# Kernel tuning notes

Hardware: AMD Instinct MI355X
Metric: run time of the kernel (lower is better)

## Reference

```python
import jax, jax.numpy as jnp
import numpy as np

N = 40000      # nodes
E = 640000     # edges
G = 64         # graphs in batch
F_IN = 128
H = 128


def setup_inputs() -> dict:
    key = jax.random.key(0)
    ks = jax.random.split(key, 10)
    x = jax.random.normal(ks[0], (N, F_IN), dtype=jnp.float32)
    edge_index = jax.random.randint(ks[1], (2, E), 0, N, dtype=jnp.int64)
    batch = jnp.sort(jax.random.randint(ks[2], (N,), 0, G, dtype=jnp.int64))
    s = 0.05
    W1 = jax.random.normal(ks[3], (F_IN, H), dtype=jnp.float32) * s
    W2 = jax.random.normal(ks[4], (H, H), dtype=jnp.float32) * s
    W3 = jax.random.normal(ks[5], (H, H), dtype=jnp.float32) * s
    Wl = jax.random.normal(ks[6], (H, 1), dtype=jnp.float32) * s
    b1 = jnp.zeros((H,), jnp.float32)
    b2 = jnp.zeros((H,), jnp.float32)
    b3 = jnp.zeros((H,), jnp.float32)
    bl = jnp.zeros((1,), jnp.float32)
    return {"x": x, "edge_index": edge_index, "batch": batch, "dropout_rate": 0,
            "W1": W1, "b1": b1, "W2": W2, "b2": b2, "W3": W3, "b3": b3,
            "Wl": Wl, "bl": bl}


def _gcn_norm(edge_index, n):
    # PyG GCNConv default: add self-loops, symmetric deg^{-1/2} normalization.
    loop = jnp.arange(n, dtype=edge_index.dtype)
    row = jnp.concatenate([edge_index[0], loop])  # source
    col = jnp.concatenate([edge_index[1], loop])  # target
    ones = jnp.ones(row.shape[0], jnp.float32)
    deg = jax.ops.segment_sum(ones, col, num_segments=n)
    dis = jnp.where(deg > 0, jax.lax.rsqrt(deg), 0.0)
    norm = dis[row] * dis[col]  # [E+N]
    return row, col, norm


def _gcn_conv(x, row, col, norm, W, b, n):
    h = x @ W + b                       # dense transform [N,H]
    msg = h[row] * norm[:, None]        # gather + scale  [E+N,H]
    return jax.ops.segment_sum(msg, col, num_segments=n)


def reference(x, edge_index, batch, dropout_rate, W1, b1, W2, b2, W3, b3, Wl, bl):
    n = x.shape[0]
    row, col, norm = _gcn_norm(edge_index, n)
    # eval mode: dropout(p=dropout_rate, training=False) is identity
    h = jax.nn.relu(_gcn_conv(x, row, col, norm, W1, b1, n))
    h = jax.nn.relu(_gcn_conv(h, row, col, norm, W2, b2, n))
    h = jax.nn.relu(_gcn_conv(h, row, col, norm, W3, b3, n))
    # global mean pool over graphs
    sums = jax.ops.segment_sum(h, batch, num_segments=G)           # [G,H]
    cnt = jax.ops.segment_sum(jnp.ones(n, jnp.float32), batch, num_segments=G)
    pooled = sums / jnp.maximum(cnt, 1.0)[:, None]
    return pooled @ Wl + bl             # [G,1]
```

## Files before the change

kernel.cpp:

```cpp
#include <hip/hip_runtime.h>

constexpr int N = 40000;
constexpr int E = 640000;
constexpr int G = 64;
constexpr int H = 128;

constexpr int NB      = (N + 255) / 256;
constexpr int EB      = (E + 255) / 256;
constexpr int GEMM1_B = N / 64;
constexpr int FUSED_B = N / 32;
constexpr int POOL_B  = N / 32;
constexpr int CSR_MAX = E + 8 * N;
constexpr int ZQ = CSR_MAX / 4 - 2;

typedef float    floatx2 __attribute__((ext_vector_type(2)));
typedef float    f32x4   __attribute__((ext_vector_type(4)));
typedef _Float16 f16x8   __attribute__((ext_vector_type(8)));

__device__ __forceinline__ unsigned pack_fp8x4(float a, float b, float c, float d) {
    unsigned v = 0;
    v = __builtin_amdgcn_cvt_pk_fp8_f32(a, b, v, false);
    v = __builtin_amdgcn_cvt_pk_fp8_f32(c, d, v, true);
    return v;
}

__device__ __forceinline__ void pk_fma(floatx2& acc, floatx2 a, floatx2 w2) {
    asm("v_pk_fma_f32 %0, %1, %2, %0" : "+v"(acc) : "v"(a), "v"(w2));
}

__device__ __forceinline__ void fma8p(floatx2& aclo, floatx2& achi, unsigned r, float w) {
    floatx2 lo = __builtin_amdgcn_cvt_pk_f32_fp8(r, false);
    floatx2 hi = __builtin_amdgcn_cvt_pk_f32_fp8(r, true);
    floatx2 w2 = {w, w};
    pk_fma(aclo, lo, w2);
    pk_fma(achi, hi, w2);
}

__device__ __forceinline__ float entry_w(int e) {
    floatx2 hi = __builtin_amdgcn_cvt_pk_f32_fp8((unsigned)e, true);
    return hi.y;
}
__device__ __forceinline__ int entry_src(int e) { return e & 0xFFFFFF; }

__device__ __forceinline__ f16x8 cvt8(float4 a, float4 b) {
    f16x8 r;
    r[0] = (_Float16)a.x; r[1] = (_Float16)a.y; r[2] = (_Float16)a.z; r[3] = (_Float16)a.w;
    r[4] = (_Float16)b.x; r[5] = (_Float16)b.y; r[6] = (_Float16)b.z; r[7] = (_Float16)b.w;
    return r;
}

__device__ __forceinline__ void aggregate_pair(const unsigned* __restrict__ h8,
                                               const int4* __restrict__ csr4,
                                               const int* __restrict__ row_ptr,
                                               const float* __restrict__ dis,
                                               int ia, int ib, int c,
                                               float4& oa, float4& ob) {
    float da = dis[ia], db = dis[ib];
    floatx2 alo = {0.f, 0.f}, ahi = {0.f, 0.f};
    floatx2 blo = {0.f, 0.f}, bhi = {0.f, 0.f};
    fma8p(alo, ahi, h8[(size_t)ia * 32 + c], da * da);
    fma8p(blo, bhi, h8[(size_t)ib * 32 + c], db * db);
    const int pa = row_ptr[ia] >> 2;
    const int na = (row_ptr[ia + 1] >> 2) - pa;
    const int pb = row_ptr[ib] >> 2;
    const int nb = (row_ptr[ib + 1] >> 2) - pb;
    const int iters = ((na > nb) ? na : nb) >> 1;

    int a0 = (0 < na) ? pa : ZQ;
    int b0 = (0 < nb) ? pb : ZQ;
    int4 ea = csr4[a0], eb = csr4[a0 + 1];
    int4 ec = csr4[b0], ed = csr4[b0 + 1];

    for (int it = 0; it < iters; ++it) {
        const int qn = (it + 1) * 2;
        const int an = (qn < na) ? pa + qn : ZQ;
        const int bn = (qn < nb) ? pb + qn : ZQ;
        int4 fa = csr4[an], fb = csr4[an + 1];
        int4 fc = csr4[bn], fd = csr4[bn + 1];

        unsigned r0 = h8[(size_t)entry_src(ea.x) * 32 + c];
        unsigned r1 = h8[(size_t)entry_src(ea.y) * 32 + c];
        unsigned r2 = h8[(size_t)entry_src(ea.z) * 32 + c];
        unsigned r3 = h8[(size_t)entry_src(ea.w) * 32 + c];
        unsigned r4 = h8[(size_t)entry_src(eb.x) * 32 + c];
        unsigned r5 = h8[(size_t)entry_src(eb.y) * 32 + c];
        unsigned r6 = h8[(size_t)entry_src(eb.z) * 32 + c];
        unsigned r7 = h8[(size_t)entry_src(eb.w) * 32 + c];
        unsigned s0 = h8[(size_t)entry_src(ec.x) * 32 + c];
        unsigned s1 = h8[(size_t)entry_src(ec.y) * 32 + c];
        unsigned s2 = h8[(size_t)entry_src(ec.z) * 32 + c];
        unsigned s3 = h8[(size_t)entry_src(ec.w) * 32 + c];
        unsigned s4 = h8[(size_t)entry_src(ed.x) * 32 + c];
        unsigned s5 = h8[(size_t)entry_src(ed.y) * 32 + c];
        unsigned s6 = h8[(size_t)entry_src(ed.z) * 32 + c];
        unsigned s7 = h8[(size_t)entry_src(ed.w) * 32 + c];

        fma8p(alo, ahi, r0, entry_w(ea.x)); fma8p(blo, bhi, s0, entry_w(ec.x));
        fma8p(alo, ahi, r1, entry_w(ea.y)); fma8p(blo, bhi, s1, entry_w(ec.y));
        fma8p(alo, ahi, r2, entry_w(ea.z)); fma8p(blo, bhi, s2, entry_w(ec.z));
        fma8p(alo, ahi, r3, entry_w(ea.w)); fma8p(blo, bhi, s3, entry_w(ec.w));
        fma8p(alo, ahi, r4, entry_w(eb.x)); fma8p(blo, bhi, s4, entry_w(ed.x));
        fma8p(alo, ahi, r5, entry_w(eb.y)); fma8p(blo, bhi, s5, entry_w(ed.y));
        fma8p(alo, ahi, r6, entry_w(eb.z)); fma8p(blo, bhi, s6, entry_w(ed.z));
        fma8p(alo, ahi, r7, entry_w(eb.w)); fma8p(blo, bhi, s7, entry_w(ed.w));

        ea = fa; eb = fb; ec = fc; ed = fd;
    }
    oa = make_float4(alo.x, alo.y, ahi.x, ahi.y);
    ob = make_float4(blo.x, blo.y, bhi.x, bhi.y);
}

__global__ void prep_wt1(const float* __restrict__ W1, _Float16* __restrict__ wt) {
    const int g  = blockIdx.x * 256 + threadIdx.x;
    const int f  = g >> 4;
    const int k0 = (g & 15) * 8;
    f16x8 v;
    #pragma unroll
    for (int j = 0; j < 8; ++j) v[j] = (_Float16)W1[(size_t)(k0 + j) * H + f];
    *reinterpret_cast<f16x8*>(wt + f * H + k0) = v;
}

__global__ __launch_bounds__(256) void gemm1_and_count(const float* __restrict__ X,
                                                       const _Float16* __restrict__ wt1,
                                                       const float* __restrict__ b,
                                                       unsigned* __restrict__ Y,
                                                       const int* __restrict__ col,
                                                       int* __restrict__ deg,
                                                       const float* __restrict__ W2,
                                                       const float* __restrict__ W3,
                                                       _Float16* __restrict__ wt) {
    __shared__ uint4 WTl[2048];
    const int blk = blockIdx.x;
    const int tid = threadIdx.x;
    if (blk >= GEMM1_B + EB) {
        const int pb = blk - (GEMM1_B + EB);
        const int m  = 1 + (pb >> 3);
        const float* W = (m == 1) ? W2 : W3;
        const int g  = (pb & 7) * 256 + tid;
        const int f  = g >> 4;
        const int k0 = (g & 15) * 8;
        f16x8 v;
        #pragma unroll
        for (int j = 0; j < 8; ++j) v[j] = (_Float16)W[(size_t)(k0 + j) * H + f];
        *reinterpret_cast<f16x8*>(wt + ((size_t)m << 14) + f * H + k0) = v;
        return;
    }
    if (blk >= GEMM1_B) {
        int e = (blk - GEMM1_B) * 256 + tid;
        if (e < E) atomicAdd(&deg[col[e]], 1);
        return;
    }
    const uint4* wtg = reinterpret_cast<const uint4*>(wt1);
    #pragma unroll
    for (int i = 0; i < 8; ++i) {
        int g = i * 256 + tid;
        WTl[g ^ ((g >> 4) & 7)] = wtg[g];
    }
    __syncthreads();

    const int lane = tid & 63;
    const int wv   = tid >> 6;
    const int c    = lane & 15;
    const int grp  = lane >> 4;
    const int node = blk * 64 + wv * 16 + c;

    const f32x4* b4 = reinterpret_cast<const f32x4*>(b);
    f32x4 acc[8];
    #pragma unroll
    for (int mt = 0; mt < 8; ++mt) acc[mt] = b4[mt * 4 + grp];

    const float4* X4 = reinterpret_cast<const float4*>(X);
    #pragma unroll
    for (int ks = 0; ks < 4; ++ks) {
        const int k0 = ks * 32 + grp * 8;
        float4 xa = X4[(size_t)node * 32 + (k0 >> 2)];
        float4 xb = X4[(size_t)node * 32 + (k0 >> 2) + 1];
        f16x8 bfr = cvt8(xa, xb);
        #pragma unroll
        for (int mt = 0; mt < 8; ++mt) {
            const int f = mt * 16 + c;
            const int g = (f << 4) + (k0 >> 3);
            f16x8 afr = *reinterpret_cast<const f16x8*>(&WTl[g ^ (f & 7)]);
            acc[mt] = __builtin_amdgcn_mfma_f32_16x16x32_f16(afr, bfr, acc[mt], 0, 0, 0);
        }
    }
    #pragma unroll
    for (int mt = 0; mt < 8; ++mt) {
        const int jg = mt * 4 + grp;
        Y[(size_t)node * 32 + jg] = pack_fp8x4(acc[mt][0], acc[mt][1], acc[mt][2], acc[mt][3]);
    }
}

__global__ void dis_block_sum(const int* __restrict__ deg, float* __restrict__ dis,
                              int* __restrict__ part) {
    __shared__ int s[256];
    int i = blockIdx.x * 256 + threadIdx.x;
    int d = (i < N) ? deg[i] : 0;
    if (i < N) dis[i] = rsqrtf((float)(d + 1));
    s[threadIdx.x] = (d + 7) & ~7;
    __syncthreads();
    for (int off = 128; off > 0; off >>= 1) {
        if (threadIdx.x < off) s[threadIdx.x] += s[threadIdx.x + off];
        __syncthreads();
    }
    if (threadIdx.x == 0) part[blockIdx.x] = s[0];
}

__global__ void scan_write(const int* __restrict__ deg, const int* __restrict__ part,
                           int* __restrict__ row_ptr, int* __restrict__ cursor) {
    __shared__ int s[256];
    const int t = threadIdx.x;
    s[t] = (t < (int)blockIdx.x) ? part[t] : 0;
    __syncthreads();
    for (int o = 128; o > 0; o >>= 1) {
        if (t < o) s[t] += s[t + o];
        __syncthreads();
    }
    const int block_off = s[0];
    __syncthreads();
    int i = blockIdx.x * 256 + t;
    int val = (i < N) ? ((deg[i] + 7) & ~7) : 0;
    s[t] = val;
    __syncthreads();
    for (int o = 1; o < 256; o <<= 1) {
        int x = (t >= o) ? s[t - o] : 0;
        __syncthreads();
        s[t] += x;
        __syncthreads();
    }
    if (i < N) {
        int excl = s[t] - val + block_off;
        row_ptr[i] = excl;
        cursor[i] = excl;
        if (i == N - 1) row_ptr[N] = excl + val;
    }
}

__global__ void fill_csr(const int* __restrict__ row, const int* __restrict__ col,
                         const float* __restrict__ dis, int* __restrict__ cursor,
                         int* __restrict__ csr) {
    int e = blockIdx.x * blockDim.x + threadIdx.x;
    if (e >= E) return;
    int r = row[e], c = col[e];
    float w = dis[r] * dis[c];
    unsigned wb = __builtin_amdgcn_cvt_pk_fp8_f32(w, 0.0f, 0, false) & 0xFFu;
    int p = atomicAdd(&cursor[c], 1);
    csr[p] = (int)((wb << 24) | (unsigned)r);
}

__global__ __launch_bounds__(256) void fused_agg_gemm(const unsigned* __restrict__ t_in,
                                                      const int4* __restrict__ csr4,
                                                      const int* __restrict__ row_ptr,
                                                      const float* __restrict__ dis,
                                                      const _Float16* __restrict__ wt,
                                                      const float* __restrict__ b,
                                                      unsigned* __restrict__ t_out) {
    __shared__ float4 tile[32 * 32];
    const int tid = threadIdx.x;
    const int node0 = blockIdx.x * 32;

    {
        const int cc = tid & 31;
        const int nl = tid >> 5;
        #pragma unroll
        for (int half = 0; half < 2; ++half) {
            const int la = half * 16 + nl;
            const int lb = la + 8;
            float4 oa, ob;
            aggregate_pair(t_in, csr4, row_ptr, dis, node0 + la, node0 + lb, cc, oa, ob);
            oa.x = fmaxf(oa.x, 0.f); oa.y = fmaxf(oa.y, 0.f);
            oa.z = fmaxf(oa.z, 0.f); oa.w = fmaxf(oa.w, 0.f);
            ob.x = fmaxf(ob.x, 0.f); ob.y = fmaxf(ob.y, 0.f);
            ob.z = fmaxf(ob.z, 0.f); ob.w = fmaxf(ob.w, 0.f);
            tile[(la * 32 + cc) ^ (la & 7)] = oa;
            tile[(lb * 32 + cc) ^ (lb & 7)] = ob;
        }
    }
    __syncthreads();

    const int lane = tid & 63;
    const int wv   = tid >> 6;
    const int c    = lane & 15;
    const int grp  = lane >> 4;

    const f32x4* b4 = reinterpret_cast<const f32x4*>(b);
    f32x4 acc00, acc01, acc10, acc11;
    acc00 = acc01 = b4[(2 * wv + 0) * 4 + grp];
    acc10 = acc11 = b4[(2 * wv + 1) * 4 + grp];

    const uint4* wtg = reinterpret_cast<const uint4*>(wt);
    #pragma unroll
    for (int ks = 0; ks < 4; ++ks) {
        const int k0 = ks * 32 + grp * 8;
        f16x8 bfr0, bfr1;
        {
            int nd = c;
            int g0 = nd * 32 + (k0 >> 2);
            float4 ta = tile[g0 ^ (nd & 7)];
            float4 tb = tile[(g0 + 1) ^ (nd & 7)];
            bfr0 = cvt8(ta, tb);
            nd = 16 + c;
            g0 = nd * 32 + (k0 >> 2);
            ta = tile[g0 ^ (nd & 7)];
            tb = tile[(g0 + 1) ^ (nd & 7)];
            bfr1 = cvt8(ta, tb);
        }
        {
            int f = (2 * wv + 0) * 16 + c;
            f16x8 afr = *reinterpret_cast<const f16x8*>(&wtg[f * 16 + (k0 >> 3)]);
            acc00 = __builtin_amdgcn_mfma_f32_16x16x32_f16(afr, bfr0, acc00, 0, 0, 0);
            acc01 = __builtin_amdgcn_mfma_f32_16x16x32_f16(afr, bfr1, acc01, 0, 0, 0);
            f = (2 * wv + 1) * 16 + c;
            afr = *reinterpret_cast<const f16x8*>(&wtg[f * 16 + (k0 >> 3)]);
            acc10 = __builtin_amdgcn_mfma_f32_16x16x32_f16(afr, bfr0, acc10, 0, 0, 0);
            acc11 = __builtin_amdgcn_mfma_f32_16x16x32_f16(afr, bfr1, acc11, 0, 0, 0);
        }
    }

    const int jg0 = (2 * wv + 0) * 4 + grp;
    const int jg1 = (2 * wv + 1) * 4 + grp;
    const int nA = node0 + c, nB = node0 + 16 + c;
    t_out[(size_t)nA * 32 + jg0] = pack_fp8x4(acc00[0], acc00[1], acc00[2], acc00[3]);
    t_out[(size_t)nB * 32 + jg0] = pack_fp8x4(acc01[0], acc01[1], acc01[2], acc01[3]);
    t_out[(size_t)nA * 32 + jg1] = pack_fp8x4(acc10[0], acc10[1], acc10[2], acc10[3]);
    t_out[(size_t)nB * 32 + jg1] = pack_fp8x4(acc11[0], acc11[1], acc11[2], acc11[3]);
}

__global__ __launch_bounds__(256) void agg_pool(const unsigned* __restrict__ t_in,
                                                const int4* __restrict__ csr4,
                                                const int* __restrict__ row_ptr,
                                                const float* __restrict__ dis,
                                                const int* __restrict__ batch,
                                                float* __restrict__ pooled) {
    __shared__ float4 tile[32 * 32];
    const int tid = threadIdx.x;
    const int c  = tid & 31;
    const int nl = tid >> 5;
    const int i0 = blockIdx.x * 32;

    #pragma unroll
    for (int half = 0; half < 2; ++half) {
        const int la = half * 16 + nl;
        const int lb = la + 8;
        float4 oa, ob;
        aggregate_pair(t_in, csr4, row_ptr, dis, i0 + la, i0 + lb, c, oa, ob);
        oa.x = fmaxf(oa.x, 0.f); oa.y = fmaxf(oa.y, 0.f);
        oa.z = fmaxf(oa.z, 0.f); oa.w = fmaxf(oa.w, 0.f);
        ob.x = fmaxf(ob.x, 0.f); ob.y = fmaxf(ob.y, 0.f);
        ob.z = fmaxf(ob.z, 0.f); ob.w = fmaxf(ob.w, 0.f);
        tile[la * 32 + c] = oa;
        tile[lb * 32 + c] = ob;
    }
    __syncthreads();

    if (tid < 128) {
        const int j = tid;
        const float* tf = reinterpret_cast<const float*>(tile);
        int cur = batch[i0];
        float s = 0.0f;
        #pragma unroll
        for (int r = 0; r < 32; ++r) {
            int g = batch[i0 + r];
            if (g != cur) { atomicAdd(&pooled[cur * H + j], s); s = 0.0f; cur = g; }
            s += tf[r * 128 + j];
        }
        atomicAdd(&pooled[cur * H + j], s);
    }
}

__global__ __launch_bounds__(128) void head(const float* __restrict__ pooled,
                                            const int* __restrict__ batch,
                                            const float* __restrict__ Wl,
                                            const float* __restrict__ bl,
                                            float* __restrict__ out) {
    const int g = blockIdx.x;
    const int j = threadIdx.x;
    __shared__ int bounds[2];
    if (j < 2) {
        int target = g + j;
        int lo = 0, hi = N;
        while (lo < hi) {
            int mid = (lo + hi) >> 1;
            if (batch[mid] < target) lo = mid + 1; else hi = mid;
        }
        bounds[j] = lo;
    }
    __syncthreads();
    float cnt = fmaxf((float)(bounds[1] - bounds[0]), 1.0f);
    float val = (pooled[g * H + j] / cnt) * Wl[j];
    __shared__ float red[128];
    red[j] = val;
    __syncthreads();
    #pragma unroll
    for (int s = 64; s > 0; s >>= 1) {
        if (j < s) red[j] += red[j + s];
        __syncthreads();
    }
    if (j == 0) out[g] = red[0] + bl[0];
}

extern "C" void kernel_launch(void* const* d_in, const int* in_sizes, int n_in,
                              void* d_out, int out_size, void* d_ws, size_t ws_size,
                              hipStream_t stream) {
    const float* x     = (const float*)d_in[0];
    const int*   ei    = (const int*)  d_in[1];
    const int*   batch = (const int*)  d_in[2];
    const float* W1 = (const float*)d_in[4];
    const float* b1 = (const float*)d_in[5];
    const float* W2 = (const float*)d_in[6];
    const float* b2 = (const float*)d_in[7];
    const float* W3 = (const float*)d_in[8];
    const float* b3 = (const float*)d_in[9];
    const float* Wl = (const float*)d_in[10];
    const float* bl = (const float*)d_in[11];
    float* out = (float*)d_out;

    const int* row = ei;
    const int* col = ei + E;

    auto align256 = [](size_t v) { return (v + 255) & ~(size_t)255; };
    char* ws = (char*)d_ws;
    size_t off = 0;
    int*   deg    = (int*)(ws + off);
    float* pooled = (float*)(deg + N);
    int*   csr    = (int*)(pooled + (size_t)G * H);
    size_t zero_bytes = (size_t)N * 4 + (size_t)G * H * 4 + (size_t)CSR_MAX * 4;
    off += align256(zero_bytes);
    float*    dis     = (float*)(ws + off); off += align256((size_t)N * 4);
    int*      row_ptr = (int*)  (ws + off); off += align256((size_t)(N + 1) * 4);
    int*      cursor  = (int*)  (ws + off); off += align256((size_t)N * 4);
    int*      part    = (int*)  (ws + off); off += align256((size_t)NB * 4);
    unsigned* bufA    = (unsigned*)(ws + off); off += align256((size_t)N * H);
    unsigned* bufB    = (unsigned*)(ws + off); off += align256((size_t)N * H);
    _Float16* wt      = (_Float16*)(ws + off); off += align256((size_t)3 * H * H * 2);
    (void)ws_size; (void)n_in; (void)in_sizes; (void)out_size;

    const int4* csr4 = reinterpret_cast<const int4*>(csr);
    _Float16* wt1 = wt;
    _Float16* wt2 = wt + (size_t)H * H;
    _Float16* wt3 = wt + (size_t)2 * H * H;

    hipMemsetAsync(deg, 0, zero_bytes, stream);
    prep_wt1<<<8, 256, 0, stream>>>(W1, wt1);
    gemm1_and_count<<<GEMM1_B + EB + 16, 256, 0, stream>>>(x, wt1, b1, bufA, col, deg,
                                                           W2, W3, wt);
    dis_block_sum<<<NB, 256, 0, stream>>>(deg, dis, part);
    scan_write<<<NB, 256, 0, stream>>>(deg, part, row_ptr, cursor);
    fill_csr<<<EB, 256, 0, stream>>>(row, col, dis, cursor, csr);
    fused_agg_gemm<<<FUSED_B, 256, 0, stream>>>(bufA, csr4, row_ptr, dis, wt2, b2, bufB);
    fused_agg_gemm<<<FUSED_B, 256, 0, stream>>>(bufB, csr4, row_ptr, dis, wt3, b3, bufA);
    agg_pool<<<POOL_B, 256, 0, stream>>>(bufA, csr4, row_ptr, dis, batch, pooled);
    head<<<G, 128, 0, stream>>>(pooled, batch, Wl, bl, out);
}
```

Baseline: 217.7 us.

## Replace scanned CSR with fixed-capacity ELL buckets filled during GEMM1

```diff
diff --git a/kernel.cpp b/kernel.cpp
--- a/kernel.cpp
+++ b/kernel.cpp
@@ -10,8 +10,10 @@
 constexpr int GEMM1_B = N / 64;
 constexpr int FUSED_B = N / 32;
 constexpr int POOL_B  = N / 32;
-constexpr int CSR_MAX = E + 8 * N;
-constexpr int ZQ = CSR_MAX / 4 - 2;
+
+constexpr int CAP   = 64;
+constexpr int CSRE  = N * CAP + 32;
+constexpr int ZQ    = N * (CAP / 4);
 
 typedef float    floatx2 __attribute__((ext_vector_type(2)));
 typedef float    f32x4   __attribute__((ext_vector_type(4)));
@@ -36,11 +38,10 @@
     pk_fma(achi, hi, w2);
 }
 
-__device__ __forceinline__ float entry_w(int e) {
-    floatx2 hi = __builtin_amdgcn_cvt_pk_f32_fp8((unsigned)e, true);
-    return hi.y;
-}
-__device__ __forceinline__ int entry_src(int e) { return e & 0xFFFFFF; }
+__device__ __forceinline__ unsigned pk16(float a, float b) {
+    auto h = __builtin_amdgcn_cvt_pkrtz(a, b);
+    return __builtin_bit_cast(unsigned, h);
+}
 
 __device__ __forceinline__ f16x8 cvt8(float4 a, float4 b) {
     f16x8 r;
@@ -49,21 +50,21 @@
     return r;
 }
 
-__device__ __forceinline__ void aggregate_pair(const unsigned* __restrict__ h8,
+__device__ __forceinline__ void aggregate_pair(const unsigned* __restrict__ h8m,
                                                const int4* __restrict__ csr4,
-                                               const int* __restrict__ row_ptr,
-                                               const float* __restrict__ dis,
+                                               const int* __restrict__ cnt,
+                                               const float* __restrict__ dis_g,
                                                int ia, int ib, int c,
                                                float4& oa, float4& ob) {
-    float da = dis[ia], db = dis[ib];
+    float da = dis_g[ia + 1], db = dis_g[ib + 1];
     floatx2 alo = {0.f, 0.f}, ahi = {0.f, 0.f};
     floatx2 blo = {0.f, 0.f}, bhi = {0.f, 0.f};
-    fma8p(alo, ahi, h8[(size_t)ia * 32 + c], da * da);
-    fma8p(blo, bhi, h8[(size_t)ib * 32 + c], db * db);
-    const int pa = row_ptr[ia] >> 2;
-    const int na = (row_ptr[ia + 1] >> 2) - pa;
-    const int pb = row_ptr[ib] >> 2;
-    const int nb = (row_ptr[ib + 1] >> 2) - pb;
+    fma8p(alo, ahi, h8m[(size_t)(ia + 1) * 32 + c], da);
+    fma8p(blo, bhi, h8m[(size_t)(ib + 1) * 32 + c], db);
+    const int na = ((cnt[ia] + 7) & ~7) >> 2;
+    const int nb = ((cnt[ib] + 7) & ~7) >> 2;
+    const int pa = ia * (CAP / 4);
+    const int pb = ib * (CAP / 4);
     const int iters = ((na > nb) ? na : nb) >> 1;
 
     int a0 = (0 < na) ? pa : ZQ;
@@ -78,40 +79,44 @@
         int4 fa = csr4[an], fb = csr4[an + 1];
         int4 fc = csr4[bn], fd = csr4[bn + 1];
 
-        unsigned r0 = h8[(size_t)entry_src(ea.x) * 32 + c];
-        unsigned r1 = h8[(size_t)entry_src(ea.y) * 32 + c];
-        unsigned r2 = h8[(size_t)entry_src(ea.z) * 32 + c];
-        unsigned r3 = h8[(size_t)entry_src(ea.w) * 32 + c];
-        unsigned r4 = h8[(size_t)entry_src(eb.x) * 32 + c];
-        unsigned r5 = h8[(size_t)entry_src(eb.y) * 32 + c];
-        unsigned r6 = h8[(size_t)entry_src(eb.z) * 32 + c];
-        unsigned r7 = h8[(size_t)entry_src(eb.w) * 32 + c];
-        unsigned s0 = h8[(size_t)entry_src(ec.x) * 32 + c];
-        unsigned s1 = h8[(size_t)entry_src(ec.y) * 32 + c];
-        unsigned s2 = h8[(size_t)entry_src(ec.z) * 32 + c];
-        unsigned s3 = h8[(size_t)entry_src(ec.w) * 32 + c];
-        unsigned s4 = h8[(size_t)entry_src(ed.x) * 32 + c];
-        unsigned s5 = h8[(size_t)entry_src(ed.y) * 32 + c];
-        unsigned s6 = h8[(size_t)entry_src(ed.z) * 32 + c];
-        unsigned s7 = h8[(size_t)entry_src(ed.w) * 32 + c];
-
-        fma8p(alo, ahi, r0, entry_w(ea.x)); fma8p(blo, bhi, s0, entry_w(ec.x));
-        fma8p(alo, ahi, r1, entry_w(ea.y)); fma8p(blo, bhi, s1, entry_w(ec.y));
-        fma8p(alo, ahi, r2, entry_w(ea.z)); fma8p(blo, bhi, s2, entry_w(ec.z));
-        fma8p(alo, ahi, r3, entry_w(ea.w)); fma8p(blo, bhi, s3, entry_w(ec.w));
-        fma8p(alo, ahi, r4, entry_w(eb.x)); fma8p(blo, bhi, s4, entry_w(ed.x));
-        fma8p(alo, ahi, r5, entry_w(eb.y)); fma8p(blo, bhi, s5, entry_w(ed.y));
-        fma8p(alo, ahi, r6, entry_w(eb.z)); fma8p(blo, bhi, s6, entry_w(ed.z));
-        fma8p(alo, ahi, r7, entry_w(eb.w)); fma8p(blo, bhi, s7, entry_w(ed.w));
+        unsigned r0 = h8m[(size_t)(unsigned)ea.x * 32 + c];
+        unsigned r1 = h8m[(size_t)(unsigned)ea.y * 32 + c];
+        unsigned r2 = h8m[(size_t)(unsigned)ea.z * 32 + c];
+        unsigned r3 = h8m[(size_t)(unsigned)ea.w * 32 + c];
+        unsigned r4 = h8m[(size_t)(unsigned)eb.x * 32 + c];
+        unsigned r5 = h8m[(size_t)(unsigned)eb.y * 32 + c];
+        unsigned r6 = h8m[(size_t)(unsigned)eb.z * 32 + c];
+        unsigned r7 = h8m[(size_t)(unsigned)eb.w * 32 + c];
+        unsigned s0 = h8m[(size_t)(unsigned)ec.x * 32 + c];
+        unsigned s1 = h8m[(size_t)(unsigned)ec.y * 32 + c];
+        unsigned s2 = h8m[(size_t)(unsigned)ec.z * 32 + c];
+        unsigned s3 = h8m[(size_t)(unsigned)ec.w * 32 + c];
+        unsigned s4 = h8m[(size_t)(unsigned)ed.x * 32 + c];
+        unsigned s5 = h8m[(size_t)(unsigned)ed.y * 32 + c];
+        unsigned s6 = h8m[(size_t)(unsigned)ed.z * 32 + c];
+        unsigned s7 = h8m[(size_t)(unsigned)ed.w * 32 + c];
+
+        fma8p(alo, ahi, r0, dis_g[ea.x]); fma8p(blo, bhi, s0, dis_g[ec.x]);
+        fma8p(alo, ahi, r1, dis_g[ea.y]); fma8p(blo, bhi, s1, dis_g[ec.y]);
+        fma8p(alo, ahi, r2, dis_g[ea.z]); fma8p(blo, bhi, s2, dis_g[ec.z]);
+        fma8p(alo, ahi, r3, dis_g[ea.w]); fma8p(blo, bhi, s3, dis_g[ec.w]);
+        fma8p(alo, ahi, r4, dis_g[eb.x]); fma8p(blo, bhi, s4, dis_g[ed.x]);
+        fma8p(alo, ahi, r5, dis_g[eb.y]); fma8p(blo, bhi, s5, dis_g[ed.y]);
+        fma8p(alo, ahi, r6, dis_g[eb.z]); fma8p(blo, bhi, s6, dis_g[ed.z]);
+        fma8p(alo, ahi, r7, dis_g[eb.w]); fma8p(blo, bhi, s7, dis_g[ed.w]);
 
         ea = fa; eb = fb; ec = fc; ed = fd;
     }
-    oa = make_float4(alo.x, alo.y, ahi.x, ahi.y);
-    ob = make_float4(blo.x, blo.y, bhi.x, bhi.y);
-}
-
-__global__ void prep_wt1(const float* __restrict__ W1, _Float16* __restrict__ wt) {
-    const int g  = blockIdx.x * 256 + threadIdx.x;
+    oa = make_float4(alo.x * da, alo.y * da, ahi.x * da, ahi.y * da);
+    ob = make_float4(blo.x * db, blo.y * db, bhi.x * db, bhi.y * db);
+}
+
+__global__ void prep_wt1(const float* __restrict__ W1, _Float16* __restrict__ wt,
+                         unsigned* __restrict__ guardA, unsigned* __restrict__ guardB) {
+    const int tid = threadIdx.x;
+    if (blockIdx.x == 0 && tid < 32) guardA[tid] = 0u;
+    if (blockIdx.x == 1 && tid < 32) guardB[tid] = 0u;
+    const int g  = blockIdx.x * 256 + tid;
     const int f  = g >> 4;
     const int k0 = (g & 15) * 8;
     f16x8 v;
@@ -120,15 +125,17 @@
     *reinterpret_cast<f16x8*>(wt + f * H + k0) = v;
 }
 
-__global__ __launch_bounds__(256) void gemm1_and_count(const float* __restrict__ X,
-                                                       const _Float16* __restrict__ wt1,
-                                                       const float* __restrict__ b,
-                                                       unsigned* __restrict__ Y,
-                                                       const int* __restrict__ col,
-                                                       int* __restrict__ deg,
-                                                       const float* __restrict__ W2,
-                                                       const float* __restrict__ W3,
-                                                       _Float16* __restrict__ wt) {
+__global__ __launch_bounds__(256) void gemm1_and_fill(const float* __restrict__ X,
+                                                      const _Float16* __restrict__ wt1,
+                                                      const float* __restrict__ b,
+                                                      unsigned* __restrict__ Y,
+                                                      const int* __restrict__ row,
+                                                      const int* __restrict__ col,
+                                                      int* __restrict__ cursor,
+                                                      int* __restrict__ csr,
+                                                      const float* __restrict__ W2,
+                                                      const float* __restrict__ W3,
+                                                      _Float16* __restrict__ wt) {
     __shared__ uint4 WTl[2048];
     const int blk = blockIdx.x;
     const int tid = threadIdx.x;
@@ -147,7 +154,11 @@
     }
     if (blk >= GEMM1_B) {
         int e = (blk - GEMM1_B) * 256 + tid;
-        if (e < E) atomicAdd(&deg[col[e]], 1);
+        if (e < E) {
+            int rsrc = row[e], cdst = col[e];
+            int p = atomicAdd(&cursor[cdst], 1);
+            if (p < CAP) csr[cdst * CAP + p] = rsrc + 1;
+        }
         return;
     }
     const uint4* wtg = reinterpret_cast<const uint4*>(wt1);
@@ -191,71 +202,20 @@
     }
 }
 
-__global__ void dis_block_sum(const int* __restrict__ deg, float* __restrict__ dis,
-                              int* __restrict__ part) {
-    __shared__ int s[256];
+__global__ void dis_pad(const int* __restrict__ cursor, float* __restrict__ dis_g) {
     int i = blockIdx.x * 256 + threadIdx.x;
-    int d = (i < N) ? deg[i] : 0;
-    if (i < N) dis[i] = rsqrtf((float)(d + 1));
-    s[threadIdx.x] = (d + 7) & ~7;
-    __syncthreads();
-    for (int off = 128; off > 0; off >>= 1) {
-        if (threadIdx.x < off) s[threadIdx.x] += s[threadIdx.x + off];
-        __syncthreads();
-    }
-    if (threadIdx.x == 0) part[blockIdx.x] = s[0];
-}
-
-__global__ void scan_write(const int* __restrict__ deg, const int* __restrict__ part,
-                           int* __restrict__ row_ptr, int* __restrict__ cursor) {
-    __shared__ int s[256];
-    const int t = threadIdx.x;
-    s[t] = (t < (int)blockIdx.x) ? part[t] : 0;
-    __syncthreads();
-    for (int o = 128; o > 0; o >>= 1) {
-        if (t < o) s[t] += s[t + o];
-        __syncthreads();
-    }
-    const int block_off = s[0];
-    __syncthreads();
-    int i = blockIdx.x * 256 + t;
-    int val = (i < N) ? ((deg[i] + 7) & ~7) : 0;
-    s[t] = val;
-    __syncthreads();
-    for (int o = 1; o < 256; o <<= 1) {
-        int x = (t >= o) ? s[t - o] : 0;
-        __syncthreads();
-        s[t] += x;
-        __syncthreads();
-    }
-    if (i < N) {
-        int excl = s[t] - val + block_off;
-        row_ptr[i] = excl;
-        cursor[i] = excl;
-        if (i == N - 1) row_ptr[N] = excl + val;
-    }
-}
-
-__global__ void fill_csr(const int* __restrict__ row, const int* __restrict__ col,
-                         const float* __restrict__ dis, int* __restrict__ cursor,
-                         int* __restrict__ csr) {
-    int e = blockIdx.x * blockDim.x + threadIdx.x;
-    if (e >= E) return;
-    int r = row[e], c = col[e];
-    float w = dis[r] * dis[c];
-    unsigned wb = __builtin_amdgcn_cvt_pk_fp8_f32(w, 0.0f, 0, false) & 0xFFu;
-    int p = atomicAdd(&cursor[c], 1);
-    csr[p] = (int)((wb << 24) | (unsigned)r);
-}
-
-__global__ __launch_bounds__(256) void fused_agg_gemm(const unsigned* __restrict__ t_in,
+    if (i < N) dis_g[i + 1] = rsqrtf((float)(cursor[i] + 1));
+    if (i == 0) dis_g[0] = 0.0f;
+}
+
+__global__ __launch_bounds__(256) void fused_agg_gemm(const unsigned* __restrict__ t_in_m,
                                                       const int4* __restrict__ csr4,
-                                                      const int* __restrict__ row_ptr,
-                                                      const float* __restrict__ dis,
+                                                      const int* __restrict__ cnt,
+                                                      const float* __restrict__ dis_g,
                                                       const _Float16* __restrict__ wt,
                                                       const float* __restrict__ b,
                                                       unsigned* __restrict__ t_out) {
-    __shared__ float4 tile[32 * 32];
+    __shared__ unsigned tile16[32 * 64];
     const int tid = threadIdx.x;
     const int node0 = blockIdx.x * 32;
 
@@ -267,13 +227,17 @@
             const int la = half * 16 + nl;
             const int lb = la + 8;
             float4 oa, ob;
-            aggregate_pair(t_in, csr4, row_ptr, dis, node0 + la, node0 + lb, cc, oa, ob);
+            aggregate_pair(t_in_m, csr4, cnt, dis_g, node0 + la, node0 + lb, cc, oa, ob);
             oa.x = fmaxf(oa.x, 0.f); oa.y = fmaxf(oa.y, 0.f);
             oa.z = fmaxf(oa.z, 0.f); oa.w = fmaxf(oa.w, 0.f);
             ob.x = fmaxf(ob.x, 0.f); ob.y = fmaxf(ob.y, 0.f);
             ob.z = fmaxf(ob.z, 0.f); ob.w = fmaxf(ob.w, 0.f);
-            tile[(la * 32 + cc) ^ (la & 7)] = oa;
-            tile[(lb * 32 + cc) ^ (lb & 7)] = ob;
+            int ua = ((la * 16 + (cc >> 1)) ^ (la & 7)) * 4 + (cc & 1) * 2;
+            tile16[ua]     = pk16(oa.x, oa.y);
+            tile16[ua + 1] = pk16(oa.z, oa.w);
+            int ub = ((lb * 16 + (cc >> 1)) ^ (lb & 7)) * 4 + (cc & 1) * 2;
+            tile16[ub]     = pk16(ob.x, ob.y);
+            tile16[ub + 1] = pk16(ob.z, ob.w);
         }
     }
     __syncthreads();
@@ -291,27 +255,18 @@
     const uint4* wtg = reinterpret_cast<const uint4*>(wt);
     #pragma unroll
     for (int ks = 0; ks < 4; ++ks) {
-        const int k0 = ks * 32 + grp * 8;
-        f16x8 bfr0, bfr1;
-        {
-            int nd = c;
-            int g0 = nd * 32 + (k0 >> 2);
-            float4 ta = tile[g0 ^ (nd & 7)];
-            float4 tb = tile[(g0 + 1) ^ (nd & 7)];
-            bfr0 = cvt8(ta, tb);
-            nd = 16 + c;
-            g0 = nd * 32 + (k0 >> 2);
-            ta = tile[g0 ^ (nd & 7)];
-            tb = tile[(g0 + 1) ^ (nd & 7)];
-            bfr1 = cvt8(ta, tb);
-        }
+        const int g8 = ks * 4 + grp;
+        const int sl0 = (c * 16 + g8) ^ (c & 7);
+        const int sl1 = ((16 + c) * 16 + g8) ^ ((16 + c) & 7);
+        f16x8 bfr0 = *reinterpret_cast<const f16x8*>(&tile16[sl0 * 4]);
+        f16x8 bfr1 = *reinterpret_cast<const f16x8*>(&tile16[sl1 * 4]);
         {
             int f = (2 * wv + 0) * 16 + c;
-            f16x8 afr = *reinterpret_cast<const f16x8*>(&wtg[f * 16 + (k0 >> 3)]);
+            f16x8 afr = *reinterpret_cast<const f16x8*>(&wtg[f * 16 + g8]);
             acc00 = __builtin_amdgcn_mfma_f32_16x16x32_f16(afr, bfr0, acc00, 0, 0, 0);
             acc01 = __builtin_amdgcn_mfma_f32_16x16x32_f16(afr, bfr1, acc01, 0, 0, 0);
             f = (2 * wv + 1) * 16 + c;
-            afr = *reinterpret_cast<const f16x8*>(&wtg[f * 16 + (k0 >> 3)]);
+            afr = *reinterpret_cast<const f16x8*>(&wtg[f * 16 + g8]);
             acc10 = __builtin_amdgcn_mfma_f32_16x16x32_f16(afr, bfr0, acc10, 0, 0, 0);
             acc11 = __builtin_amdgcn_mfma_f32_16x16x32_f16(afr, bfr1, acc11, 0, 0, 0);
         }
@@ -326,10 +281,10 @@
     t_out[(size_t)nB * 32 + jg1] = pack_fp8x4(acc11[0], acc11[1], acc11[2], acc11[3]);
 }
 
-__global__ __launch_bounds__(256) void agg_pool(const unsigned* __restrict__ t_in,
+__global__ __launch_bounds__(256) void agg_pool(const unsigned* __restrict__ t_in_m,
                                                 const int4* __restrict__ csr4,
-                                                const int* __restrict__ row_ptr,
-                                                const float* __restrict__ dis,
+                                                const int* __restrict__ cnt,
+                                                const float* __restrict__ dis_g,
                                                 const int* __restrict__ batch,
                                                 float* __restrict__ pooled) {
     __shared__ float4 tile[32 * 32];
@@ -343,7 +298,7 @@
         const int la = half * 16 + nl;
         const int lb = la + 8;
         float4 oa, ob;
-        aggregate_pair(t_in, csr4, row_ptr, dis, i0 + la, i0 + lb, c, oa, ob);
+        aggregate_pair(t_in_m, csr4, cnt, dis_g, i0 + la, i0 + lb, c, oa, ob);
         oa.x = fmaxf(oa.x, 0.f); oa.y = fmaxf(oa.y, 0.f);
         oa.z = fmaxf(oa.z, 0.f); oa.w = fmaxf(oa.w, 0.f);
         ob.x = fmaxf(ob.x, 0.f); ob.y = fmaxf(ob.y, 0.f);
@@ -421,18 +376,17 @@
     auto align256 = [](size_t v) { return (v + 255) & ~(size_t)255; };
     char* ws = (char*)d_ws;
     size_t off = 0;
-    int*   deg    = (int*)(ws + off);
-    float* pooled = (float*)(deg + N);
+    int*   cursor = (int*)(ws + off);
+    float* pooled = (float*)(cursor + N);
     int*   csr    = (int*)(pooled + (size_t)G * H);
-    size_t zero_bytes = (size_t)N * 4 + (size_t)G * H * 4 + (size_t)CSR_MAX * 4;
+    size_t zero_bytes = (size_t)N * 4 + (size_t)G * H * 4 + (size_t)CSRE * 4;
     off += align256(zero_bytes);
-    float*    dis     = (float*)(ws + off); off += align256((size_t)N * 4);
-    int*      row_ptr = (int*)  (ws + off); off += align256((size_t)(N + 1) * 4);
-    int*      cursor  = (int*)  (ws + off); off += align256((size_t)N * 4);
-    int*      part    = (int*)  (ws + off); off += align256((size_t)NB * 4);
-    unsigned* bufA    = (unsigned*)(ws + off); off += align256((size_t)N * H);
-    unsigned* bufB    = (unsigned*)(ws + off); off += align256((size_t)N * H);
-    _Float16* wt      = (_Float16*)(ws + off); off += align256((size_t)3 * H * H * 2);
+    float*    dis_g = (float*)(ws + off); off += align256((size_t)(N + 1) * 4);
+    _Float16* wt    = (_Float16*)(ws + off); off += align256((size_t)3 * H * H * 2);
+    unsigned* guardA = (unsigned*)(ws + off);
+    unsigned* bufA   = guardA + 32; off += align256(128 + (size_t)N * H);
+    unsigned* guardB = (unsigned*)(ws + off);
+    unsigned* bufB   = guardB + 32; off += align256(128 + (size_t)N * H);
     (void)ws_size; (void)n_in; (void)in_sizes; (void)out_size;
 
     const int4* csr4 = reinterpret_cast<const int4*>(csr);
@@ -440,15 +394,13 @@
     _Float16* wt2 = wt + (size_t)H * H;
     _Float16* wt3 = wt + (size_t)2 * H * H;
 
-    hipMemsetAsync(deg, 0, zero_bytes, stream);
-    prep_wt1<<<8, 256, 0, stream>>>(W1, wt1);
-    gemm1_and_count<<<GEMM1_B + EB + 16, 256, 0, stream>>>(x, wt1, b1, bufA, col, deg,
-                                                           W2, W3, wt);
-    dis_block_sum<<<NB, 256, 0, stream>>>(deg, dis, part);
-    scan_write<<<NB, 256, 0, stream>>>(deg, part, row_ptr, cursor);
-    fill_csr<<<EB, 256, 0, stream>>>(row, col, dis, cursor, csr);
-    fused_agg_gemm<<<FUSED_B, 256, 0, stream>>>(bufA, csr4, row_ptr, dis, wt2, b2, bufB);
-    fused_agg_gemm<<<FUSED_B, 256, 0, stream>>>(bufB, csr4, row_ptr, dis, wt3, b3, bufA);
-    agg_pool<<<POOL_B, 256, 0, stream>>>(bufA, csr4, row_ptr, dis, batch, pooled);
+    (void)hipMemsetAsync(cursor, 0, zero_bytes, stream);
+    prep_wt1<<<8, 256, 0, stream>>>(W1, wt1, guardA, guardB);
+    gemm1_and_fill<<<GEMM1_B + EB + 16, 256, 0, stream>>>(x, wt1, b1, bufA, row, col,
+                                                          cursor, csr, W2, W3, wt);
+    dis_pad<<<NB, 256, 0, stream>>>(cursor, dis_g);
+    fused_agg_gemm<<<FUSED_B, 256, 0, stream>>>(guardA, csr4, cursor, dis_g, wt2, b2, bufB);
+    fused_agg_gemm<<<FUSED_B, 256, 0, stream>>>(guardB, csr4, cursor, dis_g, wt3, b3, bufA);
+    agg_pool<<<POOL_B, 256, 0, stream>>>(guardA, csr4, cursor, dis_g, batch, pooled);
     head<<<G, 128, 0, stream>>>(pooled, batch, Wl, bl, out);
 }
```

Measured after the change: 242.2 us. 1.11x slower.
